# Kernel tuning notes

Hardware: AMD Instinct MI355X
Metric: run time of the kernel (lower is better)

Reference implementation:

```python
import jax, jax.numpy as jnp
import numpy as np

M = 7
KSIZE = M + 1          # kernel height = 8
PAD = KSIZE // 2       # conv padding on seq dim = 4 -> output length L+1
NUM_KERNELS = 74


def setup_inputs() -> dict:
    key = jax.random.key(0)
    kx, kk = jax.random.split(key)
    x = jax.random.normal(kx, (256, 512, 7), dtype=jnp.float32)
    kernels = jax.random.normal(kk, (NUM_KERNELS, KSIZE, 3), dtype=jnp.float32)
    return {"x": x, "kernels": kernels}


def reference(x, kernels):
    # x: (B, L, C); kernels: (74, 8, 3)
    B, L, C = x.shape
    # Width-3 conv over width-1 input with padding 1: only the middle kernel
    # column (index 1) multiplies real data; the side columns hit zero padding.
    keff = kernels[:, :, 1]  # (74, 8)
    # Seq-dim cross-correlation with padding 4 and kernel 8 -> output length L+1.
    xp = jnp.pad(x, ((0, 0), (PAD, PAD), (0, 0)))  # (B, L+8, C)
    idx = jnp.arange(L + 1)[:, None] + jnp.arange(KSIZE)[None, :]  # (L+1, 8)
    win = xp[:, idx, :]  # (B, L+1, 8, C) sliding windows
    # First 73 kernels applied to every channel; outputs ordered channel-major
    # (channel outer, kernel inner) to match the torch append order.
    out_main = jnp.einsum('btjc,kj->btck', win, keff[:NUM_KERNELS - 1])
    out_main = out_main.reshape(B, L + 1, C * (NUM_KERNELS - 1))
    # Last kernel applied to one 'random' channel; fixed to channel 0 for
    # a deterministic reference (torch uses torch.randint at runtime).
    out_last = jnp.einsum('btj,j->bt', win[:, :, :, 0], keff[NUM_KERNELS - 1])
    out = jnp.concatenate([out_main, out_last[..., None]], axis=-1)  # (B, L+1, 73*C+1)
    # Faithful to torch: reshape (L+1)*(73*C+1) elems into (B, L, -1);
    # valid because 73*C+1 == 512 is divisible by L == 512.
    return out.reshape(B, L, -1)
```

## Files before the change

kernel.cpp:

```cpp
#include <hip/hip_runtime.h>


typedef float v2f __attribute__((ext_vector_type(2)));
typedef float v4f __attribute__((ext_vector_type(4)));

#define CDIM 7
#define LDIM 512
#define TROWS 513
#define WIN_ROWS 74
#define WIN_ELEMS (WIN_ROWS * CDIM)

__global__ __launch_bounds__(256, 4) void tok_conv_kernel(
    const float* __restrict__ x,
    const float* __restrict__ kern,
    float* __restrict__ out)
{
  __shared__ float lds[WIN_ELEMS];

  const int tid  = threadIdx.x;
  const int q    = tid & 127;
  const int rpar = tid >> 7;
  const int f0   = q * 4;

  const int  cLo   = f0 / 73;
  const bool is127 = (q == 127);
  const int  cOffX = cLo;
  const int  cOffY = is127 ? 0 : (cLo < 6 ? cLo + 1 : cLo);

  v2f kP[4][8];
#pragma unroll
  for (int i = 0; i < 4; ++i) {
    const int fi = f0 + i;
    int ci, ki;
    if (fi == 511) { ci = 0; ki = 73; }
    else           { ci = fi / 73; ki = fi - 73 * ci; }
    const bool hi = (fi == 511) || (ci != cLo);
#pragma unroll
    for (int j = 0; j < 8; ++j) {
      const float kv = kern[ki * 24 + j * 3 + 1];
      kP[i][j].x = hi ? 0.f : kv;
      kP[i][j].y = hi ? kv : 0.f;
    }
  }

  const int b     = blockIdx.y;
  const int chunk = blockIdx.x;
  const float* xb = x + b * (LDIM * CDIM);

  if (chunk == 8) {
    if (rpar) return;
    const int t = 512;
    v2f w[8];
#pragma unroll
    for (int j = 0; j < 8; ++j) {
      const int p   = t + j - 4;
      const bool ok = (unsigned)p < 512u;
      const int bse = (ok ? p : 0) * CDIM;
      w[j].x = ok ? xb[bse + cOffX] : 0.f;
      w[j].y = ok ? xb[bse + cOffY] : 0.f;
    }
    v2f acc2[4] = {};
#pragma unroll
    for (int j = 0; j < 8; ++j)
#pragma unroll
      for (int i = 0; i < 4; ++i) acc2[i] += w[j] * kP[i][j];
    v4f o = {acc2[0].x + acc2[0].y, acc2[1].x + acc2[1].y,
             acc2[2].x + acc2[2].y, acc2[3].x + acc2[3].y};
    reinterpret_cast<v4f*>(out + ((size_t)b * TROWS + t) * 512)[q] = o;
    return;
  }

  const int t0 = chunk * 64;

#pragma unroll
  for (int i = tid; i < WIN_ELEMS; i += 256) {
    const int r = i / CDIM;
    const int c = i - r * CDIM;
    const int p = t0 - 4 + r;
    lds[i] = ((unsigned)p < 512u) ? xb[p * CDIM + c] : 0.f;
  }
  __syncthreads();

  const int baseX = rpar * CDIM + cOffX;
  const int baseY = rpar * CDIM + cOffY;

  v2f w[8];
#pragma unroll
  for (int j = 0; j < 8; ++j) {
    w[j].x = lds[baseX + j * CDIM];
    w[j].y = lds[baseY + j * CDIM];
  }

  v4f* orow =
      reinterpret_cast<v4f*>(out + ((size_t)b * TROWS + t0 + rpar) * 512) + q;

  int bx = baseX, by = baseY;

#pragma unroll 1
  for (int s4 = 0; s4 < 8; ++s4) {
#pragma unroll
    for (int u = 0; u < 4; ++u) {
      const int base = 2 * u;

      v2f n0, n1;
      n0.x = lds[bx + (2 * u + 8) * CDIM];
      n0.y = lds[by + (2 * u + 8) * CDIM];
      n1.x = lds[bx + (2 * u + 9) * CDIM];
      n1.y = lds[by + (2 * u + 9) * CDIM];

      v2f acc2[4] = {};
#pragma unroll
      for (int j = 0; j < 8; ++j) {
        const v2f wv = w[(base + j) & 7];
#pragma unroll
        for (int i = 0; i < 4; ++i) acc2[i] += wv * kP[i][j];
      }
      v4f o = {acc2[0].x + acc2[0].y, acc2[1].x + acc2[1].y,
               acc2[2].x + acc2[2].y, acc2[3].x + acc2[3].y};
      *orow = o;
      orow += 2 * 128;

      w[base & 7]       = n0;
      w[(base + 1) & 7] = n1;
    }
    bx += 8 * CDIM;
    by += 8 * CDIM;
  }
}

extern "C" void kernel_launch(void* const* d_in, const int* in_sizes, int n_in,
                              void* d_out, int out_size, void* d_ws, size_t ws_size,
                              hipStream_t stream) {
  const float* x    = (const float*)d_in[0];
  const float* kern = (const float*)d_in[1];
  float* out        = (float*)d_out;

  dim3 grid(9, 256);
  tok_conv_kernel<<<grid, 256, 0, stream>>>(x, kern, out);
}
```

Measured before the change: 66.96 us.

## Halve per-output FMAs by moving channel-straddling quads to the tail block

```diff
diff --git a/kernel.cpp b/kernel.cpp
--- a/kernel.cpp
+++ b/kernel.cpp
@@ -10,6 +10,9 @@
 #define WIN_ROWS 74
 #define WIN_ELEMS (WIN_ROWS * CDIM)
 
+__device__ __forceinline__ int chan_of(int f) { return (f == 511) ? 0 : (f / 73); }
+__device__ __forceinline__ int kidx_of(int f) { return (f == 511) ? 73 : (f % 73); }
+
 __global__ __launch_bounds__(256, 4) void tok_conv_kernel(
     const float* __restrict__ x,
     const float* __restrict__ kern,
@@ -17,57 +20,74 @@
 {
   __shared__ float lds[WIN_ELEMS];
 
-  const int tid  = threadIdx.x;
-  const int q    = tid & 127;
-  const int rpar = tid >> 7;
-  const int f0   = q * 4;
-
-  const int  cLo   = f0 / 73;
-  const bool is127 = (q == 127);
-  const int  cOffX = cLo;
-  const int  cOffY = is127 ? 0 : (cLo < 6 ? cLo + 1 : cLo);
-
-  v2f kP[4][8];
-#pragma unroll
-  for (int i = 0; i < 4; ++i) {
-    const int fi = f0 + i;
-    int ci, ki;
-    if (fi == 511) { ci = 0; ki = 73; }
-    else           { ci = fi / 73; ki = fi - 73 * ci; }
-    const bool hi = (fi == 511) || (ci != cLo);
-#pragma unroll
-    for (int j = 0; j < 8; ++j) {
-      const float kv = kern[ki * 24 + j * 3 + 1];
-      kP[i][j].x = hi ? 0.f : kv;
-      kP[i][j].y = hi ? kv : 0.f;
-    }
-  }
-
+  const int tid   = threadIdx.x;
   const int b     = blockIdx.y;
   const int chunk = blockIdx.x;
   const float* xb = x + b * (LDIM * CDIM);
 
   if (chunk == 8) {
-    if (rpar) return;
-    const int t = 512;
-    v2f w[8];
+    const int SQ[6] = {18, 36, 54, 91, 109, 127};
+#pragma unroll 1
+    for (int item = tid; item < 3206; item += 256) {
+      int t, qq;
+      if (item < 3078) { t = item / 6; qq = SQ[item - 6 * (item / 6)]; }
+      else             { t = 512;      qq = item - 3078; }
+      const int f0 = qq * 4;
+      const int cA = chan_of(f0);
+      const int cB = chan_of(f0 + 3);
+
+      float w0[8], w1[8];
 #pragma unroll
-    for (int j = 0; j < 8; ++j) {
-      const int p   = t + j - 4;
-      const bool ok = (unsigned)p < 512u;
-      const int bse = (ok ? p : 0) * CDIM;
-      w[j].x = ok ? xb[bse + cOffX] : 0.f;
-      w[j].y = ok ? xb[bse + cOffY] : 0.f;
+      for (int j = 0; j < 8; ++j) {
+        const int p   = t + j - 4;
+        const bool ok = (unsigned)p < 512u;
+        const int bse = (ok ? p : 0) * CDIM;
+        const float a0 = xb[bse + cA];
+        const float a1 = xb[bse + cB];
+        w0[j] = ok ? a0 : 0.f;
+        w1[j] = ok ? a1 : 0.f;
+      }
+
+      v4f o;
+#pragma unroll
+      for (int i = 0; i < 4; ++i) {
+        const int  fi   = f0 + i;
+        const int  ci   = chan_of(fi);
+        const int  ki   = kidx_of(fi);
+        const bool useB = (ci != cA);
+        float s = 0.f;
+#pragma unroll
+        for (int j = 0; j < 8; ++j) {
+          const float wv = useB ? w1[j] : w0[j];
+          s = fmaf(wv, kern[ki * 24 + j * 3 + 1], s);
+        }
+        o[i] = s;
+      }
+      reinterpret_cast<v4f*>(out + ((size_t)b * TROWS + t) * 512)[qq] = o;
     }
-    v2f acc2[4] = {};
+    return;
+  }
+
+  const int q    = tid & 127;
+  const int rpar = tid >> 7;
+  const int f0   = q * 4;
+  const int cLo  = f0 / 73;
+  const bool keep = (chan_of(f0) == chan_of(f0 + 3));
+
+  v2f kp01[8], kp23[8];
 #pragma unroll
-    for (int j = 0; j < 8; ++j)
+  for (int j = 0; j < 8; ++j) {
+    float kv[4];
 #pragma unroll
-      for (int i = 0; i < 4; ++i) acc2[i] += w[j] * kP[i][j];
-    v4f o = {acc2[0].x + acc2[0].y, acc2[1].x + acc2[1].y,
-             acc2[2].x + acc2[2].y, acc2[3].x + acc2[3].y};
-    reinterpret_cast<v4f*>(out + ((size_t)b * TROWS + t) * 512)[q] = o;
-    return;
+    for (int i = 0; i < 4; ++i) {
+      const int fi = f0 + i;
+      const int ci = chan_of(fi);
+      const int ki = kidx_of(fi);
+      const float v = kern[ki * 24 + j * 3 + 1];
+      kv[i] = (ci == cLo) ? v : 0.f;
+    }
+    kp01[j] = (v2f){kv[0], kv[1]};
+    kp23[j] = (v2f){kv[2], kv[3]};
   }
 
   const int t0 = chunk * 64;
@@ -81,20 +101,14 @@
   }
   __syncthreads();
 
-  const int baseX = rpar * CDIM + cOffX;
-  const int baseY = rpar * CDIM + cOffY;
+  int bx = rpar * CDIM + cLo;
 
-  v2f w[8];
+  float w[8];
 #pragma unroll
-  for (int j = 0; j < 8; ++j) {
-    w[j].x = lds[baseX + j * CDIM];
-    w[j].y = lds[baseY + j * CDIM];
-  }
+  for (int j = 0; j < 8; ++j) w[j] = lds[bx + j * CDIM];
 
   v4f* orow =
       reinterpret_cast<v4f*>(out + ((size_t)b * TROWS + t0 + rpar) * 512) + q;
-
-  int bx = baseX, by = baseY;
 
 #pragma unroll 1
   for (int s4 = 0; s4 < 8; ++s4) {
@@ -102,29 +116,25 @@
     for (int u = 0; u < 4; ++u) {
       const int base = 2 * u;
 
-      v2f n0, n1;
-      n0.x = lds[bx + (2 * u + 8) * CDIM];
-      n0.y = lds[by + (2 * u + 8) * CDIM];
-      n1.x = lds[bx + (2 * u + 9) * CDIM];
-      n1.y = lds[by + (2 * u + 9) * CDIM];
+      const float n0 = lds[bx + (2 * u + 8) * CDIM];
+      const float n1 = lds[bx + (2 * u + 9) * CDIM];
 
-      v2f acc2[4] = {};
+      v2f a01 = {0.f, 0.f}, a23 = {0.f, 0.f};
 #pragma unroll
       for (int j = 0; j < 8; ++j) {
-        const v2f wv = w[(base + j) & 7];
-#pragma unroll
-        for (int i = 0; i < 4; ++i) acc2[i] += wv * kP[i][j];
+        const float ws = w[(base + j) & 7];
+        const v2f wsv = {ws, ws};
+        a01 += wsv * kp01[j];
+        a23 += wsv * kp23[j];
       }
-      v4f o = {acc2[0].x + acc2[0].y, acc2[1].x + acc2[1].y,
-               acc2[2].x + acc2[2].y, acc2[3].x + acc2[3].y};
-      *orow = o;
+      const v4f o = {a01.x, a01.y, a23.x, a23.y};
+      if (keep) *orow = o;
       orow += 2 * 128;
 
       w[base & 7]       = n0;
       w[(base + 1) & 7] = n1;
     }
     bx += 8 * CDIM;
-    by += 8 * CDIM;
   }
 }
 
```

Result: slower. 114.2 us (+70.5%).
